# Kernel optimization log

Hardware: AMD Instinct MI355X
Metric: run time of the kernel (lower is better)

Reference implementation:

```python
import jax, jax.numpy as jnp
import numpy as np

S, B, T, H, K, FH, OUT = 4, 256, 256, 128, 5, 48, 1
DW, AW = 64, 32            # dynamics-MLP width, attention width
EPS_BN, EPS_U = 1e-5, 1e-6


def setup_inputs() -> dict:
    key = jax.random.key(0)
    ks = jax.random.split(key, 16)
    r = lambda i, shape, s: jax.random.normal(ks[i], shape, jnp.float32) * s
    return {
        "x": jax.random.normal(ks[0], (B, 1, T), jnp.float32),
        "t_span": jnp.linspace(0.0, 1.0, T, dtype=jnp.float32),
        # decomposer: per-scale DynamicDilationConv + BN + ReLU + Conv1d + BN + ReLU
        "c1w": r(1, (S, 1, 1, K), 0.3), "c1b": jnp.zeros((S, 1)),
        "bn1_g": jnp.ones((S, 1)), "bn1_b": jnp.zeros((S, 1)),
        "c2w": r(2, (S, 1, 1, K), 0.3), "c2b": jnp.zeros((S, 1)),
        "bn2_g": jnp.ones((S, 1)), "bn2_b": jnp.zeros((S, 1)),
        # per-scale ProbabilisticNeuralDynamics MLP: (H+1+1) -> 64 -> 2H
        "dw1": r(3, (S, H + 2, DW), 0.1), "db1": jnp.zeros((S, DW)),
        "dw2": r(4, (S, DW, 2 * H), 0.1), "db2": jnp.zeros((S, 2 * H)),
        # fusion attention H -> 32 -> 1
        "a1w": r(5, (H, AW), 0.1), "a1b": jnp.zeros((AW,)),
        "a2w": r(6, (AW, 1), 0.1), "a2b": jnp.zeros((1,)),
        # GRU (torch layout: W_ih [3H, in], W_hh [3H, H])
        "wih": r(7, (3 * H, OUT), 0.1), "whh": r(8, (3 * H, H), 0.05),
        "bih": jnp.zeros((3 * H,)), "bhh": jnp.zeros((3 * H,)),
        "fcw": r(9, (H, OUT), 0.1), "fcb": jnp.zeros((OUT,)),
        "lvw": r(10, (H, OUT), 0.1), "lvb": jnp.zeros((OUT,)),
        "init_token": jnp.zeros((1, OUT)),
    }


def _conv1d(x, w, b):
    # x:[B,C,L], w:[O,I,K]; dilation = round(clamp(exp(log_dilation=0),1)) = 1
    pad = (w.shape[-1] - 1) // 2
    y = jax.lax.conv_general_dilated(x, w, (1,), [(pad, pad)],
                                     dimension_numbers=("NCH", "OIH", "NCH"))
    return y + b[None, :, None]


def _bn(x, g, b):
    # BatchNorm1d in training mode: batch stats over (N, L)
    m = x.mean(axis=(0, 2), keepdims=True)
    v = x.var(axis=(0, 2), keepdims=True)
    return g[None, :, None] * (x - m) * jax.lax.rsqrt(v + EPS_BN) + b[None, :, None]


def _decompose(x, c1w, c1b, g1, b1, c2w, c2b, g2, b2):
    h = jnp.maximum(_bn(_conv1d(x, c1w, c1b), g1, b1), 0.0)
    h = jnp.maximum(_bn(_conv1d(h, c2w, c2b), g2, b2), 0.0)
    return h  # [B,1,T]


def _ode_scale(xseq, t_span, w1, b1, w2, b2):
    # xseq:[B,T,1]; integrate (mu, logvar) with RK4 on the t_span grid
    def f(t, h):
        idx = jnp.argmin(jnp.abs(t_span - t))
        x_t = jnp.take(xseq, idx, axis=1)                 # [B,1]
        tf = t * jnp.ones((h.shape[0], 1), h.dtype)       # time feature
        u = jnp.maximum(jnp.concatenate([h, x_t, tf], -1) @ w1 + b1, 0.0) @ w2 + b2
        return u[:, :H], u[:, H:]

    def step(carry, ts):
        h, lv = carry
        t0, t1 = ts
        dt = t1 - t0
        k1m, k1v = f(t0, h)
        k2m, k2v = f(t0 + dt / 2, h + dt / 2 * k1m)
        k3m, k3v = f(t0 + dt / 2, h + dt / 2 * k2m)
        k4m, k4v = f(t1, h + dt * k3m)
        h = h + dt / 6 * (k1m + 2 * k2m + 2 * k3m + k4m)
        lv = lv + dt / 6 * (k1v + 2 * k2v + 2 * k3v + k4v)
        return (h, lv), None

    z = jnp.zeros((xseq.shape[0], H), xseq.dtype)
    (h, lv), _ = jax.lax.scan(step, (z, z), (t_span[:-1], t_span[1:]))
    return h, lv  # final-time latent, matching h_sol[:, -1, :]


def _forward(x, t_span, c1w, c1b, bn1_g, bn1_b, c2w, c2b, bn2_g, bn2_b,
             dw1, db1, dw2, db2, a1w, a1b, a2w, a2b,
             wih, whh, bih, bhh, fcw, fcb, lvw, lvb, init_token):
    # multi-scale decomposition -> [S,B,1,T]
    comps = jax.vmap(_decompose, in_axes=(None, 0, 0, 0, 0, 0, 0, 0, 0))(
        x, c1w, c1b, bn1_g, bn1_b, c2w, c2b, bn2_g, bn2_b)
    xseqs = comps[:, :, 0, :, None]                       # [S,B,T,1]
    means, logvars = jax.vmap(_ode_scale, in_axes=(0, None, 0, 0, 0, 0))(
        xseqs, t_span, dw1, db1, dw2, db2)                # each [S,B,H]
    means = jnp.transpose(means, (1, 0, 2))               # [B,S,H]
    logvars = jnp.transpose(logvars, (1, 0, 2))
    # uncertainty-scaled attention fusion
    scores = jnp.maximum(means @ a1w + a1b, 0.0) @ a2w + a2b        # [B,S,1]
    uncert = jnp.mean(jnp.exp(logvars), axis=-1, keepdims=True)     # [B,S,1]
    weights = jax.nn.softmax(scores / (uncert + EPS_U), axis=1)
    fused = jnp.sum(weights * means, axis=1)              # [B,H]

    def dec_step(carry, _):
        h, tok = carry
        gi = tok @ wih.T + bih
        gh = h @ whh.T + bhh
        ir, iz, inn = jnp.split(gi, 3, axis=-1)
        hr, hz, hn = jnp.split(gh, 3, axis=-1)
        r = jax.nn.sigmoid(ir + hr)
        zz = jax.nn.sigmoid(iz + hz)
        n = jnp.tanh(inn + r * hn)
        h = (1.0 - zz) * n + zz * h
        pred = h @ fcw + fcb
        plv = h @ lvw + lvb
        return (h, pred), (pred, plv)

    tok0 = jnp.broadcast_to(init_token, (fused.shape[0], OUT))
    _, (outs, lvs) = jax.lax.scan(dec_step, (fused, tok0), None, length=FH)
    return jnp.transpose(outs, (1, 0, 2)), jnp.transpose(lvs, (1, 0, 2))


def reference(x, t_span, c1w, c1b, bn1_g, bn1_b, c2w, c2b, bn2_g, bn2_b,
              dw1, db1, dw2, db2, a1w, a1b, a2w, a2b,
              wih, whh, bih, bhh, fcw, fcb, lvw, lvb, init_token):
    return _forward(x, t_span, c1w, c1b, bn1_g, bn1_b, c2w, c2b, bn2_g, bn2_b,
                    dw1, db1, dw2, db2, a1w, a1b, a2w, a2b,
                    wih, whh, bih, bhh, fcw, fcb, lvw, lvb, init_token)
```

## Files before the change

kernel.cpp:

```cpp
#include <hip/hip_runtime.h>
#include <math.h>

#define NS   4
#define NB   256
#define NT   256
#define NH   128
#define NDW  64
#define NFH  48

__global__ __launch_bounds__(256) void k_d1(
    const float* __restrict__ x,
    const float* __restrict__ c1w, const float* __restrict__ c1b,
    float* __restrict__ tmpA, double* __restrict__ pp1)
{
    const int s     = blockIdx.x >> 4;
    const int chunk = blockIdx.x & 15;
    const int tid   = threadIdx.x;
    __shared__ double wred[4][2];

    float w[5];
#pragma unroll
    for (int k = 0; k < 5; ++k) w[k] = c1w[s*5 + k];
    const float cb = c1b[s];

    double ls = 0.0, lq = 0.0;
#pragma unroll 4
    for (int r = 0; r < 16; ++r) {
        const int bb = chunk*16 + r;
        const float* xb = x + bb*NT;
        float acc = cb;
#pragma unroll
        for (int k = 0; k < 5; ++k) {
            int tt = tid + k - 2;
            if (tt >= 0 && tt < NT) acc += xb[tt] * w[k];
        }
        tmpA[s*65536 + bb*NT + tid] = acc;
        ls += (double)acc; lq += (double)acc * (double)acc;
    }
#pragma unroll
    for (int off = 32; off > 0; off >>= 1) {
        ls += __shfl_xor(ls, off); lq += __shfl_xor(lq, off);
    }
    if ((tid & 63) == 0) { wred[tid>>6][0] = ls; wred[tid>>6][1] = lq; }
    __syncthreads();
    if (tid == 0) {
        pp1[(s*16 + chunk)*2 + 0] = wred[0][0]+wred[1][0]+wred[2][0]+wred[3][0];
        pp1[(s*16 + chunk)*2 + 1] = wred[0][1]+wred[1][1]+wred[2][1]+wred[3][1];
    }
}

__global__ __launch_bounds__(256) void k_d2(
    const float* __restrict__ tspan, const double* __restrict__ pp1,
    float* __restrict__ st1, int* __restrict__ imid_g, float* __restrict__ Tg)
{
    const int tid = threadIdx.x;
    __shared__ float ts[256];
    ts[tid] = tspan[tid];
    __syncthreads();
    if (tid < 255) {
        float t0 = ts[tid], t1 = ts[tid+1];
        float tm = t0 + (t1 - t0) * 0.5f;
        int best = 0; float bd = fabsf(ts[0] - tm);
        for (int j = 1; j < 256; ++j) {
            float d = fabsf(ts[j] - tm);
            if (d < bd) { bd = d; best = j; }
        }
        imid_g[tid] = best;
    }
    if (tid < 4) {
        double lsum = 0.0, lsq = 0.0;
        for (int cch = 0; cch < 16; ++cch) {
            lsum += pp1[(tid*16 + cch)*2 + 0];
            lsq  += pp1[(tid*16 + cch)*2 + 1];
        }
        const double N = 65536.0;
        double m = lsum / N;
        double v = lsq / N - m*m;
        st1[tid*2 + 0] = (float)m;
        st1[tid*2 + 1] = (float)(1.0 / sqrt(v + 1e-5));
    }
    if (tid == 4) {
        float T = 0.f;
        for (int i = 0; i < 255; ++i) T += (ts[i+1] - ts[i]);
        Tg[0] = T;
    }
}

__global__ __launch_bounds__(256) void k_d3(
    const float* __restrict__ tmpA, const float* __restrict__ st1,
    const float* __restrict__ g1,  const float* __restrict__ b1,
    const float* __restrict__ c2w, const float* __restrict__ c2b,
    float* __restrict__ cv2, double* __restrict__ pp2)
{
    const int s     = blockIdx.x >> 4;
    const int chunk = blockIdx.x & 15;
    const int tid   = threadIdx.x;
    __shared__ float hsh[256];
    __shared__ double wred[4][2];

    const float m1 = st1[s*2+0], rs1 = st1[s*2+1];
    const float A1 = g1[s]*rs1,  B1  = b1[s] - g1[s]*m1*rs1;
    float w[5];
#pragma unroll
    for (int k = 0; k < 5; ++k) w[k] = c2w[s*5 + k];
    const float cb = c2b[s];

    double ls = 0.0, lq = 0.0;
    for (int r = 0; r < 16; ++r) {
        const int bb = chunk*16 + r;
        float y = tmpA[s*65536 + bb*NT + tid];
        hsh[tid] = fmaxf(fmaf(A1, y, B1), 0.f);
        __syncthreads();
        float acc = cb;
#pragma unroll
        for (int k = 0; k < 5; ++k) {
            int tt = tid + k - 2;
            if (tt >= 0 && tt < NT) acc += hsh[tt] * w[k];
        }
        cv2[s*65536 + bb*NT + tid] = acc;
        ls += (double)acc; lq += (double)acc * (double)acc;
        __syncthreads();
    }
#pragma unroll
    for (int off = 32; off > 0; off >>= 1) {
        ls += __shfl_xor(ls, off); lq += __shfl_xor(lq, off);
    }
    if ((tid & 63) == 0) { wred[tid>>6][0] = ls; wred[tid>>6][1] = lq; }
    __syncthreads();
    if (tid == 0) {
        pp2[(s*16 + chunk)*2 + 0] = wred[0][0]+wred[1][0]+wred[2][0]+wred[3][0];
        pp2[(s*16 + chunk)*2 + 1] = wred[0][1]+wred[1][1]+wred[2][1]+wred[3][1];
    }
}

__global__ __launch_bounds__(64) void k_d4(
    const double* __restrict__ pp2, float* __restrict__ st2)
{
    const int tid = threadIdx.x;
    if (tid < 4) {
        double lsum = 0.0, lsq = 0.0;
        for (int cch = 0; cch < 16; ++cch) {
            lsum += pp2[(tid*16 + cch)*2 + 0];
            lsq  += pp2[(tid*16 + cch)*2 + 1];
        }
        const double N = 65536.0;
        double m = lsum / N;
        double v = lsq / N - m*m;
        st2[tid*2 + 0] = (float)m;
        st2[tid*2 + 1] = (float)(1.0 / sqrt(v + 1e-5));
    }
}

__global__ __launch_bounds__(64) void k_mat(
    const float* __restrict__ dw1, const float* __restrict__ dw2,
    const float* __restrict__ db2,
    float* __restrict__ Mt, float* __restrict__ bM)
{
    const int s = blockIdx.x >> 6;
    const int c = blockIdx.x & 63;
    const int k = threadIdx.x;
    __shared__ float col[128];

    col[k]      = dw1[(s*130 + k)*64 + c];
    col[k + 64] = dw1[(s*130 + 64 + k)*64 + c];
    __syncthreads();

    const float4* dp = (const float4*)(dw2 + (s*64 + k)*256);
    double acc = 0.0;
#pragma unroll 8
    for (int j4 = 0; j4 < 32; ++j4) {
        float4 dv = dp[j4];
        acc += (double)dv.x * (double)col[4*j4+0]
             + (double)dv.y * (double)col[4*j4+1]
             + (double)dv.z * (double)col[4*j4+2]
             + (double)dv.w * (double)col[4*j4+3];
    }
    Mt[(s*64 + c)*64 + k] = (float)acc;

    double pb = (double)db2[s*256 + k]      * (double)col[k]
              + (double)db2[s*256 + 64 + k] * (double)col[k + 64];
#pragma unroll
    for (int off = 32; off > 0; off >>= 1) pb += __shfl_xor(pb, off);
    if (k == 0) bM[s*64 + c] = (float)pb;
}

__device__ __forceinline__ float rlf(float v, int l) {
    return __int_as_float(__builtin_amdgcn_readlane(__float_as_int(v), l));
}
__device__ __forceinline__ float pick4f(float r0, float r1, float r2, float r3, int i) {
    int l = i & 63, h = i >> 6;
    float a = (h & 2) ? ((h & 1) ? r3 : r2) : ((h & 1) ? r1 : r0);
    return rlf(a, l);
}
__device__ __forceinline__ int pick4i(int r0, int r1, int r2, int r3, int i) {
    int l = i & 63, h = i >> 6;
    int a = (h & 2) ? ((h & 1) ? r3 : r2) : ((h & 1) ? r1 : r0);
    return __builtin_amdgcn_readlane(a, l);
}
__device__ __forceinline__ float dot64(float u1, const float* Mc, float bMc) {
    float d0 = bMc, d1 = 0.f, d2 = 0.f, d3 = 0.f;
    float cur[8], nxt[8];
#pragma unroll
    for (int k = 0; k < 8; ++k) cur[k] = rlf(u1, k);
#pragma unroll
    for (int g = 0; g < 8; ++g) {
        if (g < 7) {
#pragma unroll
            for (int k = 0; k < 8; ++k) nxt[k] = rlf(u1, 8*(g+1) + k);
        }
        d0 = fmaf(cur[0], Mc[8*g+0], d0);
        d1 = fmaf(cur[1], Mc[8*g+1], d1);
        d2 = fmaf(cur[2], Mc[8*g+2], d2);
        d3 = fmaf(cur[3], Mc[8*g+3], d3);
        d0 = fmaf(cur[4], Mc[8*g+4], d0);
        d1 = fmaf(cur[5], Mc[8*g+5], d1);
        d2 = fmaf(cur[6], Mc[8*g+6], d2);
        d3 = fmaf(cur[7], Mc[8*g+7], d3);
#pragma unroll
        for (int k = 0; k < 8; ++k) cur[k] = nxt[k];
    }
    return (d0 + d1) + (d2 + d3);
}

__global__ __attribute__((amdgpu_waves_per_eu(1, 1)))
__launch_bounds__(64) void k_ode(
    const float* __restrict__ cv2, const float* __restrict__ st2,
    const float* __restrict__ g2,  const float* __restrict__ b2,
    const float* __restrict__ tspan, const int* __restrict__ imid_g,
    const float* __restrict__ Mt, const float* __restrict__ bM_g,
    const float* __restrict__ dw1, const float* __restrict__ db1,
    float* __restrict__ S_g)
{
    const int b   = blockIdx.x;
    const int s   = b >> 8;
    const int row = b & 255;
    const int c   = threadIdx.x;

    const float m2 = st2[s*2+0], rs2 = st2[s*2+1];
    const float A2 = g2[s]*rs2,  B2  = b2[s] - g2[s]*m2*rs2;

    const float* __restrict__ xrow = cv2 + (s*NB + row)*NT;

    float ts0 = tspan[c],       ts1 = tspan[64 + c];
    float ts2 = tspan[128 + c], ts3 = tspan[192 + c];
    float xr0 = fmaxf(fmaf(A2, xrow[c],       B2), 0.f);
    float xr1 = fmaxf(fmaf(A2, xrow[64 + c],  B2), 0.f);
    float xr2 = fmaxf(fmaf(A2, xrow[128 + c], B2), 0.f);
    float xr3 = fmaxf(fmaf(A2, xrow[192 + c], B2), 0.f);
    int   im0 = imid_g[c];
    int   im1 = imid_g[64 + c];
    int   im2 = imid_g[128 + c];
    int   im3 = (192 + c < 255) ? imid_g[192 + c] : 0;

    const float bMc = bM_g[s*64 + c];
    const float b1c = db1[s*64 + c];
    const float w1x = dw1[(s*130 + 128)*64 + c];
    const float w1t = dw1[(s*130 + 129)*64 + c];

    float Mc[64];
    const float4* mp = (const float4*)(Mt + (s*64 + c)*64);
#pragma unroll
    for (int j = 0; j < 16; ++j) {
        float4 t = mp[j];
        Mc[4*j+0] = t.x; Mc[4*j+1] = t.y; Mc[4*j+2] = t.z; Mc[4*j+3] = t.w;
    }
#pragma unroll
    for (int j = 0; j < 64; ++j) asm volatile("" : "+v"(Mc[j]));

    float a = 0.f;
    float S = 0.f;

    for (int i = 0; i < 255; ++i) {
        float t0 = pick4f(ts0, ts1, ts2, ts3, i);
        float t1 = pick4f(ts0, ts1, ts2, ts3, i + 1);
        float dt = t1 - t0;
        int   im = pick4i(im0, im1, im2, im3, i);
        float xi = pick4f(xr0, xr1, xr2, xr3, i);
        float xm = pick4f(xr0, xr1, xr2, xr3, im);
        float x1 = pick4f(xr0, xr1, xr2, xr3, i + 1);
        float tm = t0 + dt * 0.5f;
        float hdt = dt * 0.5f;

        float u11 = fmaxf(a + b1c + xi*w1x + t0*w1t, 0.f);
        float v1  = dot64(u11, Mc, bMc);
        float u12 = fmaxf(fmaf(hdt, v1, a) + b1c + xm*w1x + tm*w1t, 0.f);
        float v2  = dot64(u12, Mc, bMc);
        float u13 = fmaxf(fmaf(hdt, v2, a) + b1c + xm*w1x + tm*w1t, 0.f);
        float v3  = dot64(u13, Mc, bMc);
        float u14 = fmaxf(fmaf(dt, v3, a) + b1c + x1*w1x + t1*w1t, 0.f);
        float v4  = dot64(u14, Mc, bMc);

        float d6 = dt * (1.0f / 6.0f);
        a += d6 * ((v1 + v4) + 2.f*(v2 + v3));
        S += d6 * ((u11 + u14) + 2.f*(u12 + u13));
    }

    S_g[(s*256 + row)*64 + c] = S;
}

__global__ __launch_bounds__(384, 1) void k_gru(
    const float* __restrict__ S_g, const float* __restrict__ dw2,
    const float* __restrict__ db2, const float* __restrict__ Tg,
    const float* __restrict__ a1w, const float* __restrict__ a1b,
    const float* __restrict__ a2w, const float* __restrict__ a2b,
    const float* __restrict__ wih, const float* __restrict__ whh,
    const float* __restrict__ bih, const float* __restrict__ bhh,
    const float* __restrict__ fcw, const float* __restrict__ fcb,
    const float* __restrict__ lvw, const float* __restrict__ lvb,
    const float* __restrict__ init_token, float* __restrict__ out)
{
    const int b   = blockIdx.x;
    const int tid = threadIdx.x;

    __shared__ __align__(16) float Ssh[4][64];
    __shared__ __align__(16) float msh[4][128];
    __shared__ __align__(16) float evs[4][128];
    __shared__ __align__(16) float hl[128];
    __shared__ float ghl[384];
    __shared__ float scoreL[4];
    __shared__ float unc_part[2][4];
    __shared__ float wgt[4];
    __shared__ float redL[2][2];
    __shared__ float tokL;

    if (tid < 256) {
        int s = tid >> 6, cc = tid & 63;
        Ssh[s][cc] = S_g[(s*256 + b)*64 + cc];
    }
    const float T = Tg[0];
    __syncthreads();

    for (int e = tid; e < 1024; e += 384) {
        int s = e >> 8, j = e & 255;
        float acc = T * db2[s*256 + j];
        const float4* s4 = (const float4*)Ssh[s];
#pragma unroll
        for (int k4 = 0; k4 < 16; ++k4) {
            float4 sv = s4[k4];
            acc += sv.x * dw2[(s*64 + 4*k4 + 0)*256 + j]
                 + sv.y * dw2[(s*64 + 4*k4 + 1)*256 + j]
                 + sv.z * dw2[(s*64 + 4*k4 + 2)*256 + j]
                 + sv.w * dw2[(s*64 + 4*k4 + 3)*256 + j];
        }
        if (j < 128) msh[s][j] = acc;
        else         evs[s][j - 128] = expf(acc);
    }
    __syncthreads();

    if (tid < 128) {
        int wv = tid >> 6;
#pragma unroll
        for (int s = 0; s < 4; ++s) {
            float v = evs[s][tid];
#pragma unroll
            for (int off = 32; off > 0; off >>= 1) v += __shfl_xor(v, off);
            if ((tid & 63) == 0) unc_part[wv][s] = v;
        }
    }
    if (tid < 128) {
        int s = tid >> 5, aq = tid & 31;
        float hd = a1b[aq];
#pragma unroll 4
        for (int i = 0; i < 128; ++i) hd += msh[s][i] * a1w[i*32 + aq];
        hd = fmaxf(hd, 0.f);
        float sc = hd * a2w[aq];
#pragma unroll
        for (int off = 16; off > 0; off >>= 1) sc += __shfl_xor(sc, off);
        if (aq == 0) scoreL[s] = sc + a2b[0];
    }
    __syncthreads();
    if (tid == 0) {
        float sv[4], mx = -1e30f;
#pragma unroll
        for (int s = 0; s < 4; ++s) {
            float u = (unc_part[0][s] + unc_part[1][s]) / 128.f;
            sv[s] = scoreL[s] / (u + 1e-6f);
            mx = fmaxf(mx, sv[s]);
        }
        float se = 0.f, ev[4];
#pragma unroll
        for (int s = 0; s < 4; ++s) { ev[s] = expf(sv[s] - mx); se += ev[s]; }
#pragma unroll
        for (int s = 0; s < 4; ++s) wgt[s] = ev[s] / se;
        tokL = init_token[0];
    }
    __syncthreads();
    if (tid < 128) {
        float f = 0.f;
#pragma unroll
        for (int s = 0; s < 4; ++s) f += wgt[s] * msh[s][tid];
        hl[tid] = f;
    }

    float4 whh4[32];
    const float4* wr = (const float4*)(whh + tid*128);
#pragma unroll
    for (int k = 0; k < 32; ++k) whh4[k] = wr[k];
    float bhhj = bhh[tid];
    float wih_r = 0.f, wih_z = 0.f, wih_n = 0.f;
    float bih_r = 0.f, bih_z = 0.f, bih_n = 0.f;
    float fcwi = 0.f, lvwi = 0.f;
    if (tid < 128) {
        wih_r = wih[tid]; wih_z = wih[128+tid]; wih_n = wih[256+tid];
        bih_r = bih[tid]; bih_z = bih[128+tid]; bih_n = bih[256+tid];
        fcwi  = fcw[tid]; lvwi  = lvw[tid];
    }
    const float fcbv = fcb[0], lvbv = lvb[0];
    __syncthreads();

    for (int t = 0; t < NFH; ++t) {
        float g0 = 0.f, g1 = 0.f, g2 = 0.f, g3 = 0.f;
        const float4* h4 = (const float4*)hl;
#pragma unroll
        for (int k = 0; k < 32; ++k) {
            float4 hv = h4[k];
            float4 wvv = whh4[k];
            g0 += hv.x * wvv.x; g1 += hv.y * wvv.y;
            g2 += hv.z * wvv.z; g3 += hv.w * wvv.w;
        }
        ghl[tid] = ((g0 + g1) + (g2 + g3)) + bhhj;
        __syncthreads();

        if (tid < 128) {
            float tok = tokL;
            float r  = 1.f / (1.f + expf(-(tok*wih_r + bih_r + ghl[tid])));
            float zz = 1.f / (1.f + expf(-(tok*wih_z + bih_z + ghl[128+tid])));
            float n  = tanhf(tok*wih_n + bih_n + r * ghl[256+tid]);
            float hn = (1.f - zz) * n + zz * hl[tid];
            hl[tid] = hn;
            float pp = hn * fcwi, pl = hn * lvwi;
#pragma unroll
            for (int off = 32; off > 0; off >>= 1) {
                pp += __shfl_xor(pp, off);
                pl += __shfl_xor(pl, off);
            }
            int wvx = tid >> 6;
            if ((tid & 63) == 0) { redL[wvx][0] = pp; redL[wvx][1] = pl; }
        }
        __syncthreads();
        if (tid == 0) {
            float pr = redL[0][0] + redL[1][0] + fcbv;
            float pv = redL[0][1] + redL[1][1] + lvbv;
            out[b*NFH + t] = pr;
            out[NB*NFH + b*NFH + t] = pv;
            tokL = pr;
        }
        __syncthreads();
    }
}

extern "C" void kernel_launch(void* const* d_in, const int* in_sizes, int n_in,
                              void* d_out, int out_size, void* d_ws, size_t ws_size,
                              hipStream_t stream)
{
    const float* x      = (const float*)d_in[0];
    const float* tspan  = (const float*)d_in[1];
    const float* c1w    = (const float*)d_in[2];
    const float* c1b    = (const float*)d_in[3];
    const float* bn1g   = (const float*)d_in[4];
    const float* bn1b   = (const float*)d_in[5];
    const float* c2w    = (const float*)d_in[6];
    const float* c2b    = (const float*)d_in[7];
    const float* bn2g   = (const float*)d_in[8];
    const float* bn2b   = (const float*)d_in[9];
    const float* dw1    = (const float*)d_in[10];
    const float* db1    = (const float*)d_in[11];
    const float* dw2    = (const float*)d_in[12];
    const float* db2    = (const float*)d_in[13];
    const float* a1w    = (const float*)d_in[14];
    const float* a1b    = (const float*)d_in[15];
    const float* a2w    = (const float*)d_in[16];
    const float* a2b    = (const float*)d_in[17];
    const float* wih    = (const float*)d_in[18];
    const float* whh    = (const float*)d_in[19];
    const float* bih    = (const float*)d_in[20];
    const float* bhh    = (const float*)d_in[21];
    const float* fcw    = (const float*)d_in[22];
    const float* fcb    = (const float*)d_in[23];
    const float* lvw    = (const float*)d_in[24];
    const float* lvb    = (const float*)d_in[25];
    const float* itok   = (const float*)d_in[26];

    float* ws    = (float*)d_ws;
    float*  cv2  = ws;
    float*  tmpA = ws + 262144;
    float*  S_g  = ws + 524288;
    float*  Mt   = ws + 589824;
    float*  bMg  = ws + 606208;
    float*  Tg   = ws + 606464;
    int*    imid = (int*)(ws + 606720);
    double* pp1  = (double*)(ws + 606976);
    double* pp2  = (double*)(ws + 607232);
    float*  st1  = ws + 607488;
    float*  st2  = ws + 607496;

    k_d1<<<64, 256, 0, stream>>>(x, c1w, c1b, tmpA, pp1);
    k_d2<<<1, 256, 0, stream>>>(tspan, pp1, st1, imid, Tg);
    k_d3<<<64, 256, 0, stream>>>(tmpA, st1, bn1g, bn1b, c2w, c2b, cv2, pp2);
    k_d4<<<1, 64, 0, stream>>>(pp2, st2);
    k_mat<<<256, 64, 0, stream>>>(dw1, dw2, db2, Mt, bMg);
    k_ode<<<1024, 64, 0, stream>>>(cv2, st2, bn2g, bn2b, tspan, imid,
                                   Mt, bMg, dw1, db1, S_g);
    k_gru<<<256, 384, 0, stream>>>(S_g, dw2, db2, Tg, a1w, a1b, a2w, a2b,
                                   wih, whh, bih, bhh, fcw, fcb, lvw, lvb,
                                   itok, (float*)d_out);
}
```

Before: 366.6 us.

## Fold BN stat kernels into consumers, widen decomposer grids, use LDS dot in ODE

Removes the single-block k_d2 and k_d4 kernels: BN statistics are now reduced redundantly by each consumer block from 64 per-chunk partials, and the time-grid midpoint search moves into an extra block of k_mat. The decomposer kernels run with 256 blocks of 4 rows each instead of 64 blocks of 16 rows, for better occupancy. In the ODE loop the per-step 64-wide matvec broadcasts the hidden vector through LDS with float4 reads instead of 64 readlane operations. The LDS writes and reads inside the single-wave loop carry no barrier, so correctness relies on wavefront-synchronous execution, and every block now repeats the statistic reduction.

Measured after the change: 421.5 us. +15.0%, slower.

```diff
diff --git a/kernel.cpp b/kernel.cpp
--- a/kernel.cpp
+++ b/kernel.cpp
@@ -13,8 +13,8 @@
     const float* __restrict__ c1w, const float* __restrict__ c1b,
     float* __restrict__ tmpA, double* __restrict__ pp1)
 {
-    const int s     = blockIdx.x >> 4;
-    const int chunk = blockIdx.x & 15;
+    const int s     = blockIdx.x >> 6;
+    const int chunk = blockIdx.x & 63;
     const int tid   = threadIdx.x;
     __shared__ double wred[4][2];
 
@@ -24,9 +24,9 @@
     const float cb = c1b[s];
 
     double ls = 0.0, lq = 0.0;
-#pragma unroll 4
-    for (int r = 0; r < 16; ++r) {
-        const int bb = chunk*16 + r;
+#pragma unroll
+    for (int r = 0; r < 4; ++r) {
+        const int bb = chunk*4 + r;
         const float* xb = x + bb*NT;
         float acc = cb;
 #pragma unroll
@@ -44,70 +44,42 @@
     if ((tid & 63) == 0) { wred[tid>>6][0] = ls; wred[tid>>6][1] = lq; }
     __syncthreads();
     if (tid == 0) {
-        pp1[(s*16 + chunk)*2 + 0] = wred[0][0]+wred[1][0]+wred[2][0]+wred[3][0];
-        pp1[(s*16 + chunk)*2 + 1] = wred[0][1]+wred[1][1]+wred[2][1]+wred[3][1];
-    }
-}
-
-__global__ __launch_bounds__(256) void k_d2(
-    const float* __restrict__ tspan, const double* __restrict__ pp1,
-    float* __restrict__ st1, int* __restrict__ imid_g, float* __restrict__ Tg)
-{
-    const int tid = threadIdx.x;
-    __shared__ float ts[256];
-    ts[tid] = tspan[tid];
-    __syncthreads();
-    if (tid < 255) {
-        float t0 = ts[tid], t1 = ts[tid+1];
-        float tm = t0 + (t1 - t0) * 0.5f;
-        int best = 0; float bd = fabsf(ts[0] - tm);
-        for (int j = 1; j < 256; ++j) {
-            float d = fabsf(ts[j] - tm);
-            if (d < bd) { bd = d; best = j; }
-        }
-        imid_g[tid] = best;
-    }
-    if (tid < 4) {
-        double lsum = 0.0, lsq = 0.0;
-        for (int cch = 0; cch < 16; ++cch) {
-            lsum += pp1[(tid*16 + cch)*2 + 0];
-            lsq  += pp1[(tid*16 + cch)*2 + 1];
-        }
-        const double N = 65536.0;
-        double m = lsum / N;
-        double v = lsq / N - m*m;
-        st1[tid*2 + 0] = (float)m;
-        st1[tid*2 + 1] = (float)(1.0 / sqrt(v + 1e-5));
-    }
-    if (tid == 4) {
-        float T = 0.f;
-        for (int i = 0; i < 255; ++i) T += (ts[i+1] - ts[i]);
-        Tg[0] = T;
+        pp1[(s*64 + chunk)*2 + 0] = wred[0][0]+wred[1][0]+wred[2][0]+wred[3][0];
+        pp1[(s*64 + chunk)*2 + 1] = wred[0][1]+wred[1][1]+wred[2][1]+wred[3][1];
     }
 }
 
 __global__ __launch_bounds__(256) void k_d3(
-    const float* __restrict__ tmpA, const float* __restrict__ st1,
+    const float* __restrict__ tmpA, const double* __restrict__ pp1,
     const float* __restrict__ g1,  const float* __restrict__ b1,
     const float* __restrict__ c2w, const float* __restrict__ c2b,
     float* __restrict__ cv2, double* __restrict__ pp2)
 {
-    const int s     = blockIdx.x >> 4;
-    const int chunk = blockIdx.x & 15;
+    const int s     = blockIdx.x >> 6;
+    const int chunk = blockIdx.x & 63;
     const int tid   = threadIdx.x;
     __shared__ float hsh[256];
     __shared__ double wred[4][2];
 
-    const float m1 = st1[s*2+0], rs1 = st1[s*2+1];
-    const float A1 = g1[s]*rs1,  B1  = b1[s] - g1[s]*m1*rs1;
+    double lsum = 0.0, lsq = 0.0;
+    for (int q = 0; q < 64; ++q) {
+        lsum += pp1[(s*64 + q)*2 + 0];
+        lsq  += pp1[(s*64 + q)*2 + 1];
+    }
+    const double Nn = 65536.0;
+    double mm = lsum / Nn;
+    double vv = lsq / Nn - mm*mm;
+    const float m1 = (float)mm, rs1 = (float)(1.0 / sqrt(vv + 1e-5));
+    const float A1 = g1[s]*rs1, B1 = b1[s] - g1[s]*m1*rs1;
+
     float w[5];
 #pragma unroll
     for (int k = 0; k < 5; ++k) w[k] = c2w[s*5 + k];
     const float cb = c2b[s];
 
     double ls = 0.0, lq = 0.0;
-    for (int r = 0; r < 16; ++r) {
-        const int bb = chunk*16 + r;
+    for (int r = 0; r < 4; ++r) {
+        const int bb = chunk*4 + r;
         float y = tmpA[s*65536 + bb*NT + tid];
         hsh[tid] = fmaxf(fmaf(A1, y, B1), 0.f);
         __syncthreads();
@@ -128,34 +100,39 @@
     if ((tid & 63) == 0) { wred[tid>>6][0] = ls; wred[tid>>6][1] = lq; }
     __syncthreads();
     if (tid == 0) {
-        pp2[(s*16 + chunk)*2 + 0] = wred[0][0]+wred[1][0]+wred[2][0]+wred[3][0];
-        pp2[(s*16 + chunk)*2 + 1] = wred[0][1]+wred[1][1]+wred[2][1]+wred[3][1];
-    }
-}
-
-__global__ __launch_bounds__(64) void k_d4(
-    const double* __restrict__ pp2, float* __restrict__ st2)
-{
-    const int tid = threadIdx.x;
-    if (tid < 4) {
-        double lsum = 0.0, lsq = 0.0;
-        for (int cch = 0; cch < 16; ++cch) {
-            lsum += pp2[(tid*16 + cch)*2 + 0];
-            lsq  += pp2[(tid*16 + cch)*2 + 1];
-        }
-        const double N = 65536.0;
-        double m = lsum / N;
-        double v = lsq / N - m*m;
-        st2[tid*2 + 0] = (float)m;
-        st2[tid*2 + 1] = (float)(1.0 / sqrt(v + 1e-5));
+        pp2[(s*64 + chunk)*2 + 0] = wred[0][0]+wred[1][0]+wred[2][0]+wred[3][0];
+        pp2[(s*64 + chunk)*2 + 1] = wred[0][1]+wred[1][1]+wred[2][1]+wred[3][1];
     }
 }
 
 __global__ __launch_bounds__(64) void k_mat(
     const float* __restrict__ dw1, const float* __restrict__ dw2,
-    const float* __restrict__ db2,
-    float* __restrict__ Mt, float* __restrict__ bM)
-{
+    const float* __restrict__ db2, const float* __restrict__ tspan,
+    float* __restrict__ Mt, float* __restrict__ bM,
+    int* __restrict__ imid_g, float* __restrict__ Tg)
+{
+    if (blockIdx.x == 256) {
+        __shared__ float ts[256];
+        const int t = threadIdx.x;
+        for (int e = t; e < 256; e += 64) ts[e] = tspan[e];
+        __syncthreads();
+        for (int i = t; i < 255; i += 64) {
+            float t0 = ts[i], t1 = ts[i+1];
+            float tm = t0 + (t1 - t0) * 0.5f;
+            int best = 0; float bd = fabsf(ts[0] - tm);
+            for (int j = 1; j < 256; ++j) {
+                float d = fabsf(ts[j] - tm);
+                if (d < bd) { bd = d; best = j; }
+            }
+            imid_g[i] = best;
+        }
+        if (t == 0) {
+            float T = 0.f;
+            for (int i = 0; i < 255; ++i) T += (ts[i+1] - ts[i]);
+            Tg[0] = T;
+        }
+        return;
+    }
     const int s = blockIdx.x >> 6;
     const int c = blockIdx.x & 63;
     const int k = threadIdx.x;
@@ -197,34 +174,25 @@
     int a = (h & 2) ? ((h & 1) ? r3 : r2) : ((h & 1) ? r1 : r0);
     return __builtin_amdgcn_readlane(a, l);
 }
-__device__ __forceinline__ float dot64(float u1, const float* Mc, float bMc) {
+__device__ __forceinline__ float dot64_lds(const float* __restrict__ u1s,
+                                           const float* __restrict__ Mc,
+                                           float bMc) {
     float d0 = bMc, d1 = 0.f, d2 = 0.f, d3 = 0.f;
-    float cur[8], nxt[8];
-#pragma unroll
-    for (int k = 0; k < 8; ++k) cur[k] = rlf(u1, k);
-#pragma unroll
-    for (int g = 0; g < 8; ++g) {
-        if (g < 7) {
-#pragma unroll
-            for (int k = 0; k < 8; ++k) nxt[k] = rlf(u1, 8*(g+1) + k);
-        }
-        d0 = fmaf(cur[0], Mc[8*g+0], d0);
-        d1 = fmaf(cur[1], Mc[8*g+1], d1);
-        d2 = fmaf(cur[2], Mc[8*g+2], d2);
-        d3 = fmaf(cur[3], Mc[8*g+3], d3);
-        d0 = fmaf(cur[4], Mc[8*g+4], d0);
-        d1 = fmaf(cur[5], Mc[8*g+5], d1);
-        d2 = fmaf(cur[6], Mc[8*g+6], d2);
-        d3 = fmaf(cur[7], Mc[8*g+7], d3);
-#pragma unroll
-        for (int k = 0; k < 8; ++k) cur[k] = nxt[k];
+    const float4* up = (const float4*)u1s;
+#pragma unroll
+    for (int g = 0; g < 16; ++g) {
+        float4 uv = up[g];
+        d0 = fmaf(uv.x, Mc[4*g+0], d0);
+        d1 = fmaf(uv.y, Mc[4*g+1], d1);
+        d2 = fmaf(uv.z, Mc[4*g+2], d2);
+        d3 = fmaf(uv.w, Mc[4*g+3], d3);
     }
     return (d0 + d1) + (d2 + d3);
 }
 
 __global__ __attribute__((amdgpu_waves_per_eu(1, 1)))
 __launch_bounds__(64) void k_ode(
-    const float* __restrict__ cv2, const float* __restrict__ st2,
+    const float* __restrict__ cv2, const double* __restrict__ pp2,
     const float* __restrict__ g2,  const float* __restrict__ b2,
     const float* __restrict__ tspan, const int* __restrict__ imid_g,
     const float* __restrict__ Mt, const float* __restrict__ bM_g,
@@ -236,8 +204,18 @@
     const int row = b & 255;
     const int c   = threadIdx.x;
 
-    const float m2 = st2[s*2+0], rs2 = st2[s*2+1];
-    const float A2 = g2[s]*rs2,  B2  = b2[s] - g2[s]*m2*rs2;
+    __shared__ __align__(16) float u1s[64];
+
+    double lsum = 0.0, lsq = 0.0;
+    for (int q = 0; q < 64; ++q) {
+        lsum += pp2[(s*64 + q)*2 + 0];
+        lsq  += pp2[(s*64 + q)*2 + 1];
+    }
+    const double Nn = 65536.0;
+    double mm = lsum / Nn;
+    double vv = lsq / Nn - mm*mm;
+    const float m2 = (float)mm, rs2 = (float)(1.0 / sqrt(vv + 1e-5));
+    const float A2 = g2[s]*rs2, B2 = b2[s] - g2[s]*m2*rs2;
 
     const float* __restrict__ xrow = cv2 + (s*NB + row)*NT;
 
@@ -282,13 +260,20 @@
         float hdt = dt * 0.5f;
 
         float u11 = fmaxf(a + b1c + xi*w1x + t0*w1t, 0.f);
-        float v1  = dot64(u11, Mc, bMc);
+        u1s[c] = u11;
+        float v1  = dot64_lds(u1s, Mc, bMc);
+
         float u12 = fmaxf(fmaf(hdt, v1, a) + b1c + xm*w1x + tm*w1t, 0.f);
-        float v2  = dot64(u12, Mc, bMc);
+        u1s[c] = u12;
+        float v2  = dot64_lds(u1s, Mc, bMc);
+
         float u13 = fmaxf(fmaf(hdt, v2, a) + b1c + xm*w1x + tm*w1t, 0.f);
-        float v3  = dot64(u13, Mc, bMc);
+        u1s[c] = u13;
+        float v3  = dot64_lds(u1s, Mc, bMc);
+
         float u14 = fmaxf(fmaf(dt, v3, a) + b1c + x1*w1x + t1*w1t, 0.f);
-        float v4  = dot64(u14, Mc, bMc);
+        u1s[c] = u14;
+        float v4  = dot64_lds(u1s, Mc, bMc);
 
         float d6 = dt * (1.0f / 6.0f);
         a += d6 * ((v1 + v4) + 2.f*(v2 + v3));
@@ -490,16 +475,12 @@
     float*  Tg   = ws + 606464;
     int*    imid = (int*)(ws + 606720);
     double* pp1  = (double*)(ws + 606976);
-    double* pp2  = (double*)(ws + 607232);
-    float*  st1  = ws + 607488;
-    float*  st2  = ws + 607496;
-
-    k_d1<<<64, 256, 0, stream>>>(x, c1w, c1b, tmpA, pp1);
-    k_d2<<<1, 256, 0, stream>>>(tspan, pp1, st1, imid, Tg);
-    k_d3<<<64, 256, 0, stream>>>(tmpA, st1, bn1g, bn1b, c2w, c2b, cv2, pp2);
-    k_d4<<<1, 64, 0, stream>>>(pp2, st2);
-    k_mat<<<256, 64, 0, stream>>>(dw1, dw2, db2, Mt, bMg);
-    k_ode<<<1024, 64, 0, stream>>>(cv2, st2, bn2g, bn2b, tspan, imid,
+    double* pp2  = (double*)(ws + 608000);
+
+    k_d1<<<256, 256, 0, stream>>>(x, c1w, c1b, tmpA, pp1);
+    k_mat<<<257, 64, 0, stream>>>(dw1, dw2, db2, tspan, Mt, bMg, imid, Tg);
+    k_d3<<<256, 256, 0, stream>>>(tmpA, pp1, bn1g, bn1b, c2w, c2b, cv2, pp2);
+    k_ode<<<1024, 64, 0, stream>>>(cv2, pp2, bn2g, bn2b, tspan, imid,
                                    Mt, bMg, dw1, db1, S_g);
     k_gru<<<256, 384, 0, stream>>>(S_g, dw2, db2, Tg, a1w, a1b, a2w, a2b,
                                    wih, whh, bih, bhh, fcw, fcb, lvw, lvb,
```
